# Kernel optimization log

Hardware: AMD Instinct MI355X
Metric: run time of the kernel (lower is better)

## Reference

```python
import jax, jax.numpy as jnp
import numpy as np

V, E, H, K = 50000, 256, 256, 16   # vocab, embed_dim, bi_lstm_hidden, n_tags (E must equal H)
HD = H // 2                        # per-direction hidden
B, NSEG, S = 32, 8, 128            # batch, segments, segment size
T = NSEG * S


def _lstm_dir(x, mask, Wih, Whh, b, h0, c0, reverse):
    """Masked (packed-equivalent) unidirectional LSTM. x:[T,B,E], mask:[T,B]."""
    def step(carry, inp):
        h, c = carry
        xt, mt = inp
        g = xt @ Wih.T + h @ Whh.T + b
        i, f, gg, o = jnp.split(g, 4, axis=-1)  # torch gate order i,f,g,o
        cn = jax.nn.sigmoid(f) * c + jax.nn.sigmoid(i) * jnp.tanh(gg)
        hn = jax.nn.sigmoid(o) * jnp.tanh(cn)
        m = mt[:, None]
        return (jnp.where(m, hn, h), jnp.where(m, cn, c)), jnp.where(m, hn, 0.0)
    (hT, cT), out = jax.lax.scan(step, (h0, c0), (x, mask), reverse=reverse)
    return out, (hT, cT)


def _bilstm(x, lengths, pf, pb, init=None):
    """pack_padded_sequence-equivalent BiLSTM. x:[T,B,E], lengths:[B]."""
    Tt, Bb = x.shape[0], x.shape[1]
    mask = jnp.arange(Tt)[:, None] < lengths[None, :]
    z = jnp.zeros((Bb, HD), x.dtype)
    h0f, c0f, h0b, c0b = init if init is not None else (z, z, z, z)
    of, (hf, cf) = _lstm_dir(x, mask, pf[0], pf[1], pf[2], h0f, c0f, False)
    ob, (hb, cb) = _lstm_dir(x, mask, pb[0], pb[1], pb[2], h0b, c0b, True)
    return jnp.concatenate([of, ob], -1), (hf, cf, hb, cb)


def _viterbi(emission, mask, start, trans, end):
    """torchcrf-style masked Viterbi decode. emission:[T,B,K], mask:[T,B]."""
    score = start[None, :] + emission[0]  # [B,K]
    def step(sc, inp):
        em, m = inp
        allsc = sc[:, :, None] + trans[None, :, :] + em[:, None, :]  # [B,K,K]
        best = jnp.max(allsc, axis=1)
        idx = jnp.argmax(allsc, axis=1).astype(jnp.int32)
        return jnp.where(m[:, None], best, sc), idx
    final, hist = jax.lax.scan(step, score, (emission[1:], mask[1:]))
    final = final + end[None, :]
    best_score = jnp.max(final, axis=-1)                 # [B]
    last = jnp.argmax(final, axis=-1).astype(jnp.int32)  # [B]
    def back(cur, inp):
        h, m = inp  # h:[B,K] backpointers at step t, m = mask[t+1]
        prev = jnp.take_along_axis(h, cur[:, None], axis=1)[:, 0]
        cur = jnp.where(m, prev, cur)
        return cur, cur
    _, tags_rev = jax.lax.scan(back, last, (hist, mask[1:]), reverse=True)
    tags = jnp.concatenate([tags_rev, last[None]], axis=0)  # [T,B]
    return tags, best_score


def _forward(texts, lengths, emb_table, Wih_f, Whh_f, bih_f, bhh_f,
             Wih_b, Whh_b, bih_b, bhh_b, Wlin, blin,
             crf_start, crf_trans, crf_end):
    pf = (Wih_f, Whh_f, bih_f + bhh_f)
    pb = (Wih_b, Whh_b, bih_b + bhh_b)
    emb = emb_table[texts]                      # [B,NSEG,S,E]
    x = jnp.transpose(emb, (1, 2, 0, 3))        # [NSEG,S,B,E]
    lens_seg = lengths.T                        # [NSEG,B]
    # pass 1: independent BiLSTM per segment (zero init state)
    outs, hids = jax.vmap(lambda xs, ls: _bilstm(xs, ls, pf, pb))(x, lens_seg)
    # positions >= per-segment max length are the raw embeddings (torch.cat with pad_text)
    maxlen = jnp.max(lens_seg, axis=1)          # [NSEG]
    over = jnp.arange(S)[None, :, None] >= maxlen[:, None, None]  # [NSEG,S,1]
    outs = jnp.where(over[..., None], x, outs)  # relies on E == 2*HD == H
    lstm1 = outs.reshape(NSEG * S, B, H)        # torch.cat(outputs, dim=0) -> [T,B,H]
    # get_text_lengths: per sample, valid tokens of all segments first, then pad tokens
    t_idx = jnp.arange(T)
    seg, pos = t_idx // S, t_idx % S
    valid = pos[None, :] < lengths[:, seg]                 # [B,T]
    key2 = jnp.where(valid, t_idx[None, :], t_idx[None, :] + T)
    perm = jnp.argsort(key2, axis=1)                       # [B,T] stable reorder
    lstm1_bt = jnp.transpose(lstm1, (1, 0, 2))             # [B,T,H]
    lstm2_in = jnp.transpose(
        jnp.take_along_axis(lstm1_bt, perm[..., None], axis=1), (1, 0, 2))  # [T,B,H]
    new_len = jnp.sum(lengths, axis=1)                     # [B]
    # pass 2: same LSTM weights, init state = final hidden of LAST segment (self.hidden)
    hf, cf, hb, cb = hids
    init = (hf[-1], cf[-1], hb[-1], cb[-1])
    lstm2_out, _ = _bilstm(lstm2_in, new_len, pf, pb, init)
    emission = lstm2_out @ Wlin.T + blin[None, None, :]    # [T,B,K]
    mask = jnp.arange(T)[:, None] < new_len[None, :]       # [T,B]
    return _viterbi(emission, mask, crf_start, crf_trans, crf_end)


def setup_inputs() -> dict:
    key = jax.random.key(0)
    ks = jax.random.split(key, 16)
    def u(k, shape, n):
        s = 1.0 / np.sqrt(n)
        return jax.random.uniform(k, shape, jnp.float32, -s, s)
    return {
        "texts": jax.random.randint(ks[0], (B, NSEG, S), 0, V).astype(jnp.int32),
        "lengths": jax.random.randint(ks[1], (B, NSEG), 1, S + 1).astype(jnp.int32),
        "emb_table": jax.random.normal(ks[2], (V, E), jnp.float32),
        "Wih_f": u(ks[3], (4 * HD, E), HD), "Whh_f": u(ks[4], (4 * HD, HD), HD),
        "bih_f": u(ks[5], (4 * HD,), HD), "bhh_f": u(ks[6], (4 * HD,), HD),
        "Wih_b": u(ks[7], (4 * HD, E), HD), "Whh_b": u(ks[8], (4 * HD, HD), HD),
        "bih_b": u(ks[9], (4 * HD,), HD), "bhh_b": u(ks[10], (4 * HD,), HD),
        "Wlin": u(ks[11], (K, H), H), "blin": u(ks[12], (K,), H),
        "crf_start": jax.random.uniform(ks[13], (K,), jnp.float32, -0.1, 0.1),
        "crf_trans": jax.random.uniform(ks[14], (K, K), jnp.float32, -0.1, 0.1),
        "crf_end": jax.random.uniform(ks[15], (K,), jnp.float32, -0.1, 0.1),
    }


def reference(texts, lengths, emb_table, Wih_f, Whh_f, bih_f, bhh_f,
              Wih_b, Whh_b, bih_b, bhh_b, Wlin, blin,
              crf_start, crf_trans, crf_end):
    # returns (tags [T,B] int32 padded with last tag beyond each length, viterbi score [B])
    return _forward(texts, lengths, emb_table, Wih_f, Whh_f, bih_f, bhh_f,
                    Wih_b, Whh_b, bih_b, bhh_b, Wlin, blin,
                    crf_start, crf_trans, crf_end)
```

## Files before the change

kernel.cpp:

```cpp
#include <hip/hip_runtime.h>
#include <cstdint>
#include <cstddef>


#define B_    32
#define NSEG_ 8
#define S_    128
#define T_    1024
#define E_    256
#define HD_   128
#define G_    512
#define K_    16
#define KS_   8

#define PIN4(v) asm volatile("" : "+v"((v).x), "+v"((v).y), "+v"((v).z), "+v"((v).w))

__global__ void prep_kernel(const int* __restrict__ lengths,
                            int* __restrict__ seg_off, int* __restrict__ new_len,
                            const float* __restrict__ bih_f, const float* __restrict__ bhh_f,
                            const float* __restrict__ bih_b, const float* __restrict__ bhh_b,
                            float* __restrict__ bias1,
                            const float* __restrict__ Wih_f, const float* __restrict__ Wih_b,
                            float* __restrict__ WT1)
{
    int gtid = blockIdx.x * blockDim.x + threadIdx.x;
    if (gtid < B_) {
        int acc = 0;
        for (int s = 0; s < NSEG_; s++) { seg_off[gtid*NSEG_ + s] = acc; acc += lengths[gtid*NSEG_ + s]; }
        new_len[gtid] = acc;
    }
    if (gtid < 512)       bias1[gtid] = bih_f[gtid] + bhh_f[gtid];
    else if (gtid < 1024) bias1[gtid] = bih_b[gtid-512] + bhh_b[gtid-512];
    for (int e = gtid; e < 256*1024; e += gridDim.x * blockDim.x) {
        int k = e >> 10, j = e & 1023;
        WT1[e] = (j < 512) ? Wih_f[j*E_ + k] : Wih_b[(j-512)*E_ + k];
    }
}

template <int MODE>
__global__ void __launch_bounds__(256, 4)
proj_kernel(const int* __restrict__ texts, const float* __restrict__ emb,
            const float* __restrict__ WT1, const float* __restrict__ bias1,
            const float* __restrict__ lstm_packed, float* __restrict__ xproj,
            const int* __restrict__ seg_off, const int* __restrict__ new_len)
{
    int b  = blockIdx.z;
    int nl = new_len[b];
    int p0 = blockIdx.x * 32;
    if (p0 >= nl) return;
    int j0 = blockIdx.y * 256;

    __shared__ __align__(16) float As[32][256];
    __shared__ const float* rowp[32];
    int tid = threadIdx.x;
    if (tid < 32) {
        int p = p0 + tid;
        const float* r = emb;
        if (p < nl) {
            if (MODE == 0) {
                int sg = 0;
                #pragma unroll
                for (int q = 1; q < NSEG_; q++) if (seg_off[b*NSEG_ + q] <= p) sg = q;
                int t   = p - seg_off[b*NSEG_ + sg];
                int tok = texts[(b*NSEG_ + sg)*S_ + t];
                r = emb + (size_t)tok * E_;
            } else {
                r = lstm_packed + ((size_t)b*T_ + p) * 256;
            }
        }
        rowp[tid] = r;
    }
    __syncthreads();
    #pragma unroll 4
    for (int i = 0; i < 32; i++) As[i][tid] = rowp[i][tid];
    __syncthreads();

    int pg = tid >> 6;
    int jg = tid & 63;
    int j  = j0 + jg*4;
    float acc[8][4];
    #pragma unroll
    for (int i = 0; i < 8; i++) { acc[i][0]=0.f; acc[i][1]=0.f; acc[i][2]=0.f; acc[i][3]=0.f; }

    const float* wbase = WT1 + j;
    for (int k = 0; k < 256; k += 4) {
        float4 w0 = *(const float4*)(wbase + (size_t)(k+0)*1024);
        float4 w1 = *(const float4*)(wbase + (size_t)(k+1)*1024);
        float4 w2 = *(const float4*)(wbase + (size_t)(k+2)*1024);
        float4 w3 = *(const float4*)(wbase + (size_t)(k+3)*1024);
        #pragma unroll
        for (int i = 0; i < 8; i++) {
            float4 a = *(const float4*)&As[pg*8 + i][k];
            acc[i][0] = fmaf(a.w, w3.x, fmaf(a.z, w2.x, fmaf(a.y, w1.x, fmaf(a.x, w0.x, acc[i][0]))));
            acc[i][1] = fmaf(a.w, w3.y, fmaf(a.z, w2.y, fmaf(a.y, w1.y, fmaf(a.x, w0.y, acc[i][1]))));
            acc[i][2] = fmaf(a.w, w3.z, fmaf(a.z, w2.z, fmaf(a.y, w1.z, fmaf(a.x, w0.z, acc[i][2]))));
            acc[i][3] = fmaf(a.w, w3.w, fmaf(a.z, w2.w, fmaf(a.y, w1.w, fmaf(a.x, w0.w, acc[i][3]))));
        }
    }
    float4 bs = *(const float4*)(bias1 + j);
    #pragma unroll
    for (int i = 0; i < 8; i++) {
        int p = p0 + pg*8 + i;
        if (p < nl) {
            float4 r;
            r.x = acc[i][0] + bs.x; r.y = acc[i][1] + bs.y;
            r.z = acc[i][2] + bs.z; r.w = acc[i][3] + bs.w;
            *(float4*)(xproj + (((size_t)b*T_ + p) << 10) + j) = r;
        }
    }
}

__device__ __forceinline__ float sig_f(float x) { return 1.0f / (1.0f + __expf(-x)); }
__device__ __forceinline__ float tanh_f(float x) {
    float xc = fminf(fmaxf(x, -15.0f), 15.0f);
    float e  = __expf(-2.0f * xc);
    return (1.0f - e) / (1.0f + e);
}

__device__ __forceinline__ void lstm_chain(
    const float* __restrict__ Whh,
    const float* __restrict__ xp,
    float* __restrict__ outp,
    int p_base, int len, int dir, int rev,
    const float* __restrict__ h0, const float* __restrict__ c0,
    float* __restrict__ hT, float* __restrict__ cT)
{
    __shared__ __align__(16) float  h_sh[HD_];
    __shared__ __align__(16) float4 psum[4*HD_];
    int t = threadIdx.x;
    int j = t & 127, q = t >> 7;

    float4 w[4][8];
    #pragma unroll
    for (int g = 0; g < 4; g++) {
        const float4* wr = (const float4*)(Whh + (size_t)(j + 128*g) * HD_ + 32*q);
        #pragma unroll
        for (int i = 0; i < 8; i++) { w[g][i] = wr[i]; PIN4(w[g][i]); }
    }

    float c_reg = 0.0f;
    if (t < HD_) {
        h_sh[t] = h0 ? h0[t] : 0.0f;
        c_reg   = c0 ? c0[t] : 0.0f;
    }
    __syncthreads();

    const float* xcol = xp + dir * G_ + j;
    const int    oco  = dir * HD_ + j;

    float xvi[KS_], xvf[KS_], xvg[KS_], xvo[KS_], hbuf[KS_];

    for (int gs = 0; gs < len; gs += KS_) {
        if (t < HD_) {
            if (gs > 0) {
                #pragma unroll
                for (int u = 0; u < KS_; u++) {
                    int s = gs - KS_ + u;
                    int p = p_base + (rev ? (len - 1 - s) : s);
                    outp[(size_t)p * 256 + oco] = hbuf[u];
                }
            }
            #pragma unroll
            for (int u = 0; u < KS_; u++) {
                int s = gs + u;
                if (s < len) {
                    int p = p_base + (rev ? (len - 1 - s) : s);
                    const float* r = xcol + ((size_t)p << 10);
                    xvi[u] = r[0]; xvf[u] = r[128]; xvg[u] = r[256]; xvo[u] = r[384];
                }
            }
        }
        #pragma unroll
        for (int u = 0; u < KS_; u++) {
            if (gs + u < len) {
                const float4* hv = (const float4*)h_sh + q * 8;
                float4 a0 = make_float4(0.f,0.f,0.f,0.f);
                float4 a1 = a0, a2 = a0, a3 = a0;
                #pragma unroll
                for (int i = 0; i < 8; i++) {
                    float4 h4 = hv[i];
                    a0.x = fmaf(h4.x, w[0][i].x, a0.x); a0.y = fmaf(h4.y, w[0][i].y, a0.y);
                    a0.z = fmaf(h4.z, w[0][i].z, a0.z); a0.w = fmaf(h4.w, w[0][i].w, a0.w);
                    a1.x = fmaf(h4.x, w[1][i].x, a1.x); a1.y = fmaf(h4.y, w[1][i].y, a1.y);
                    a1.z = fmaf(h4.z, w[1][i].z, a1.z); a1.w = fmaf(h4.w, w[1][i].w, a1.w);
                    a2.x = fmaf(h4.x, w[2][i].x, a2.x); a2.y = fmaf(h4.y, w[2][i].y, a2.y);
                    a2.z = fmaf(h4.z, w[2][i].z, a2.z); a2.w = fmaf(h4.w, w[2][i].w, a2.w);
                    a3.x = fmaf(h4.x, w[3][i].x, a3.x); a3.y = fmaf(h4.y, w[3][i].y, a3.y);
                    a3.z = fmaf(h4.z, w[3][i].z, a3.z); a3.w = fmaf(h4.w, w[3][i].w, a3.w);
                }
                psum[q*128 + j] = make_float4((a0.x+a0.y)+(a0.z+a0.w),
                                              (a1.x+a1.y)+(a1.z+a1.w),
                                              (a2.x+a2.y)+(a2.z+a2.w),
                                              (a3.x+a3.y)+(a3.z+a3.w));
                __syncthreads();
                if (t < HD_) {
                    float4 p0 = psum[j], p1 = psum[128 + j], p2 = psum[256 + j], p3 = psum[384 + j];
                    float gi = xvi[u] + ((p0.x + p1.x) + (p2.x + p3.x));
                    float gf = xvf[u] + ((p0.y + p1.y) + (p2.y + p3.y));
                    float gg = xvg[u] + ((p0.z + p1.z) + (p2.z + p3.z));
                    float go = xvo[u] + ((p0.w + p1.w) + (p2.w + p3.w));
                    float cn = sig_f(gf) * c_reg + sig_f(gi) * tanh_f(gg);
                    c_reg = cn;
                    float hn = sig_f(go) * tanh_f(cn);
                    h_sh[j] = hn;
                    hbuf[u] = hn;
                }
                __syncthreads();
            }
        }
    }
    if (t < HD_ && len > 0) {
        int gs = ((len - 1) / KS_) * KS_;
        #pragma unroll
        for (int u = 0; u < KS_; u++) {
            int s = gs + u;
            if (s < len) {
                int p = p_base + (rev ? (len - 1 - s) : s);
                outp[(size_t)p * 256 + oco] = hbuf[u];
            }
        }
    }
    if (hT != nullptr && t < HD_) { hT[t] = h_sh[t]; cT[t] = c_reg; }
}

__global__ void __launch_bounds__(512, 2)
lstm1_kernel(const int* __restrict__ lengths, const int* __restrict__ seg_off,
             const float* __restrict__ Whh_f, const float* __restrict__ Whh_b,
             const float* __restrict__ xproj, float* __restrict__ lstm_packed,
             float* __restrict__ hinit, float* __restrict__ cinit)
{
    int cid = blockIdx.x;
    int b = cid >> 4, seg = (cid >> 1) & 7, dir = cid & 1;
    int len = lengths[b*NSEG_ + seg];
    int pb  = seg_off[b*NSEG_ + seg];
    const float* Whh = dir ? Whh_b : Whh_f;
    float* hT = nullptr; float* cT = nullptr;
    if (seg == NSEG_ - 1) {
        hT = hinit + (dir*B_ + b)*HD_;
        cT = cinit + (dir*B_ + b)*HD_;
    }
    lstm_chain(Whh, xproj + ((size_t)b << 20), lstm_packed + (size_t)b*T_*256,
               pb, len, dir, dir, nullptr, nullptr, hT, cT);
}

__global__ void __launch_bounds__(512, 2)
lstm2_kernel(const int* __restrict__ new_len,
             const float* __restrict__ Whh_f, const float* __restrict__ Whh_b,
             const float* __restrict__ xproj, float* __restrict__ lstm_packed,
             const float* __restrict__ hinit, const float* __restrict__ cinit)
{
    int cid = blockIdx.x;
    int b = cid >> 1, dir = cid & 1;
    int len = new_len[b];
    const float* Whh = dir ? Whh_b : Whh_f;
    lstm_chain(Whh, xproj + ((size_t)b << 20), lstm_packed + (size_t)b*T_*256,
               0, len, dir, dir,
               hinit + (dir*B_ + b)*HD_, cinit + (dir*B_ + b)*HD_,
               nullptr, nullptr);
}

__global__ void __launch_bounds__(256)
emission_kernel(const float* __restrict__ lstm_packed, const float* __restrict__ Wlin,
                const float* __restrict__ blin, float* __restrict__ emis,
                const int* __restrict__ new_len)
{
    int b  = blockIdx.y;
    int nl = new_len[b];
    int p0 = blockIdx.x * 16;
    if (p0 >= nl) return;
    int pl = threadIdx.x >> 4, s = threadIdx.x & 15;
    int p  = p0 + pl;
    const float4* xr = (const float4*)(lstm_packed + ((size_t)b*T_ + p) * 256);
    const float4* wr = (const float4*)(Wlin + (size_t)s * 256);
    float ax = 0.f, ay = 0.f, az = 0.f, aw = 0.f;
    #pragma unroll
    for (int i = 0; i < 64; i++) {
        float4 a = xr[i]; float4 ww = wr[i];
        ax = fmaf(a.x, ww.x, ax); ay = fmaf(a.y, ww.y, ay);
        az = fmaf(a.z, ww.z, az); aw = fmaf(a.w, ww.w, aw);
    }
    if (p < nl) emis[((size_t)b*T_ + p)*K_ + s] = (ax + ay) + (az + aw) + blin[s];
}

__global__ void __launch_bounds__(64)
viterbi_kernel(const float* __restrict__ emis, const float* __restrict__ start,
               const float* __restrict__ trans, const float* __restrict__ endv,
               const int* __restrict__ new_len, float* __restrict__ out)
{
    int b    = blockIdx.x;
    int nl   = new_len[b];
    int lane = threadIdx.x;
    int s    = lane & 15, q4 = lane >> 4;

    __shared__ unsigned char hist[T_ * K_];
    __shared__ unsigned char tagb[T_];

    float tr[4];
    #pragma unroll
    for (int jj = 0; jj < 4; jj++) tr[jj] = trans[(q4*4 + jj)*K_ + s];

    const float* em = emis + (size_t)b * T_ * K_;
    float sc = start[s] + em[s];

    for (int p = 1; p < nl; p++) {
        float e = em[p*K_ + s];
        float m = -3.4e38f; int a = 0;
        #pragma unroll
        for (int jj = 0; jj < 4; jj++) {
            int q   = q4*4 + jj;
            float sq = __shfl(sc, q, 16);
            float v  = sq + tr[jj];
            if (v > m) { m = v; a = q; }
        }
        #pragma unroll
        for (int d = 16; d < 64; d <<= 1) {
            float mo = __shfl_xor(m, d);
            int   ao = __shfl_xor(a, d);
            if (mo > m || (mo == m && ao < a)) { m = mo; a = ao; }
        }
        sc = m + e;
        if (lane < K_) hist[p*K_ + s] = (unsigned char)a;
    }

    float m = sc + endv[s]; int a = s;
    #pragma unroll
    for (int d = 1; d < 16; d <<= 1) {
        float mo = __shfl_xor(m, d);
        int   ao = __shfl_xor(a, d);
        if (mo > m || (mo == m && ao < a)) { m = mo; a = ao; }
    }
    int last = a;
    if (lane == 0) out[T_*B_ + b] = m;
    __syncthreads();

    for (int i = lane; i < T_; i += 64) tagb[i] = (unsigned char)last;
    __syncthreads();
    if (lane == 0) {
        int cur = last;
        for (int j = nl - 2; j >= 0; j--) {
            cur = hist[(j+1)*K_ + cur];
            tagb[j] = (unsigned char)cur;
        }
    }
    __syncthreads();
    for (int i = lane; i < T_; i += 64) out[(size_t)i*B_ + b] = (float)tagb[i];
}

extern "C" void kernel_launch(void* const* d_in, const int* in_sizes, int n_in,
                              void* d_out, int out_size, void* d_ws, size_t ws_size,
                              hipStream_t stream)
{
    (void)in_sizes; (void)n_in; (void)out_size; (void)ws_size;
    const int*   texts   = (const int*)  d_in[0];
    const int*   lengths = (const int*)  d_in[1];
    const float* emb     = (const float*)d_in[2];
    const float* Wih_f   = (const float*)d_in[3];
    const float* Whh_f   = (const float*)d_in[4];
    const float* bih_f   = (const float*)d_in[5];
    const float* bhh_f   = (const float*)d_in[6];
    const float* Wih_b   = (const float*)d_in[7];
    const float* Whh_b   = (const float*)d_in[8];
    const float* bih_b   = (const float*)d_in[9];
    const float* bhh_b   = (const float*)d_in[10];
    const float* Wlin    = (const float*)d_in[11];
    const float* blin    = (const float*)d_in[12];
    const float* c_start = (const float*)d_in[13];
    const float* c_trans = (const float*)d_in[14];
    const float* c_end   = (const float*)d_in[15];
    float* out = (float*)d_out;

    char* w = (char*)d_ws;
    int*   seg_off     = (int*)(w);
    int*   new_len     = (int*)(w + 1024);
    float* bias1       = (float*)(w + 4096);
    float* WT1         = (float*)(w + 8192);
    float* hinit       = (float*)(w + 8192 + 1048576);
    float* cinit       = hinit + 8192;
    float* lstm_packed = cinit + 8192;
    float* xproj       = lstm_packed + (size_t)B_*T_*256;
    float* emis        = xproj + ((size_t)B_ << 20);

    prep_kernel<<<128, 256, 0, stream>>>(lengths, seg_off, new_len,
                                         bih_f, bhh_f, bih_b, bhh_b, bias1,
                                         Wih_f, Wih_b, WT1);
    proj_kernel<0><<<dim3(32, 4, B_), 256, 0, stream>>>(texts, emb, WT1, bias1,
                                                        lstm_packed, xproj, seg_off, new_len);
    lstm1_kernel<<<512, 512, 0, stream>>>(lengths, seg_off, Whh_f, Whh_b,
                                          xproj, lstm_packed, hinit, cinit);
    proj_kernel<1><<<dim3(32, 4, B_), 256, 0, stream>>>(texts, emb, WT1, bias1,
                                                        lstm_packed, xproj, seg_off, new_len);
    lstm2_kernel<<<64, 512, 0, stream>>>(new_len, Whh_f, Whh_b,
                                         xproj, lstm_packed, hinit, cinit);
    emission_kernel<<<dim3(64, B_), 256, 0, stream>>>(lstm_packed, Wlin, blin, emis, new_len);
    viterbi_kernel<<<B_, 64, 0, stream>>>(emis, c_start, c_trans, c_end, new_len, out);
}
```

Before: 1.582 ms.

## Interleave gate columns and prefetch next chunk of input projections in LSTM

The gate layout of the input projection weights and bias is permuted so the four gates of each hidden unit are contiguous, which lets the recurrent loop fetch all four gate inputs with a single 16-byte load. Loads for the next chunk of time steps are issued ahead with inline assembly and waited on by explicit vmcnt counters, so their latency overlaps the current chunk's serial compute. Hidden outputs are now stored immediately at each step rather than buffered. This relies on hand-managed waitcnt ordering, where a wrong count could read stale registers.

```diff
diff --git a/kernel.cpp b/kernel.cpp
--- a/kernel.cpp
+++ b/kernel.cpp
@@ -15,6 +15,17 @@
 
 #define PIN4(v) asm volatile("" : "+v"((v).x), "+v"((v).y), "+v"((v).z), "+v"((v).w))
 
+__device__ __forceinline__ float4 gload4(const float* p) {
+    float4 d;
+    asm volatile("global_load_dwordx4 %0, %1, off"
+                 : "=v"(d) : "v"((unsigned long long)(uintptr_t)p));
+    return d;
+}
+__device__ __forceinline__ void gstore1(float* p, float v) {
+    asm volatile("global_store_dword %0, %1, off"
+                 :: "v"((unsigned long long)(uintptr_t)p), "v"(v));
+}
+
 __global__ void prep_kernel(const int* __restrict__ lengths,
                             int* __restrict__ seg_off, int* __restrict__ new_len,
                             const float* __restrict__ bih_f, const float* __restrict__ bhh_f,
@@ -29,11 +40,16 @@
         for (int s = 0; s < NSEG_; s++) { seg_off[gtid*NSEG_ + s] = acc; acc += lengths[gtid*NSEG_ + s]; }
         new_len[gtid] = acc;
     }
-    if (gtid < 512)       bias1[gtid] = bih_f[gtid] + bhh_f[gtid];
-    else if (gtid < 1024) bias1[gtid] = bih_b[gtid-512] + bhh_b[gtid-512];
+    if (gtid < 1024) {
+        int dir = gtid >> 9, w = gtid & 511, j = w >> 2, g = w & 3;
+        int r = g * HD_ + j;
+        bias1[gtid] = dir ? (bih_b[r] + bhh_b[r]) : (bih_f[r] + bhh_f[r]);
+    }
     for (int e = gtid; e < 256*1024; e += gridDim.x * blockDim.x) {
-        int k = e >> 10, j = e & 1023;
-        WT1[e] = (j < 512) ? Wih_f[j*E_ + k] : Wih_b[(j-512)*E_ + k];
+        int k = e >> 10, jcol = e & 1023;
+        int dir = jcol >> 9, w = jcol & 511, j = w >> 2, g = w & 3;
+        int r = g * HD_ + j;
+        WT1[e] = dir ? Wih_b[(size_t)r*E_ + k] : Wih_f[(size_t)r*E_ + k];
     }
 }
 
@@ -145,28 +161,31 @@
     }
     __syncthreads();
 
-    const float* xcol = xp + dir * G_ + j;
-    const int    oco  = dir * HD_ + j;
-
-    float xvi[KS_], xvf[KS_], xvg[KS_], xvo[KS_], hbuf[KS_];
+    const float* xbase = xp + dir * G_ + 4 * j;
+    float*       obase = outp + dir * HD_ + j;
+
+    float4 xc[KS_], xn[KS_];
+
+    if (t < HD_ && len > 0) {
+        #pragma unroll
+        for (int u = 0; u < KS_; u++) {
+            int s = u < len ? u : len - 1;
+            int p = p_base + (rev ? (len - 1 - s) : s);
+            xn[u] = gload4(xbase + ((size_t)p << 10));
+        }
+    }
+    asm volatile("s_waitcnt vmcnt(0)");
 
     for (int gs = 0; gs < len; gs += KS_) {
         if (t < HD_) {
-            if (gs > 0) {
+            #pragma unroll
+            for (int u = 0; u < KS_; u++) { PIN4(xn[u]); xc[u] = xn[u]; }
+            if (gs + KS_ < len) {
                 #pragma unroll
                 for (int u = 0; u < KS_; u++) {
-                    int s = gs - KS_ + u;
+                    int s = gs + KS_ + u; s = s < len ? s : len - 1;
                     int p = p_base + (rev ? (len - 1 - s) : s);
-                    outp[(size_t)p * 256 + oco] = hbuf[u];
-                }
-            }
-            #pragma unroll
-            for (int u = 0; u < KS_; u++) {
-                int s = gs + u;
-                if (s < len) {
-                    int p = p_base + (rev ? (len - 1 - s) : s);
-                    const float* r = xcol + ((size_t)p << 10);
-                    xvi[u] = r[0]; xvf[u] = r[128]; xvg[u] = r[256]; xvo[u] = r[384];
+                    xn[u] = gload4(xbase + ((size_t)p << 10));
                 }
             }
         }
@@ -195,32 +214,25 @@
                 __syncthreads();
                 if (t < HD_) {
                     float4 p0 = psum[j], p1 = psum[128 + j], p2 = psum[256 + j], p3 = psum[384 + j];
-                    float gi = xvi[u] + ((p0.x + p1.x) + (p2.x + p3.x));
-                    float gf = xvf[u] + ((p0.y + p1.y) + (p2.y + p3.y));
-                    float gg = xvg[u] + ((p0.z + p1.z) + (p2.z + p3.z));
-                    float go = xvo[u] + ((p0.w + p1.w) + (p2.w + p3.w));
+                    float gi = xc[u].x + ((p0.x + p1.x) + (p2.x + p3.x));
+                    float gf = xc[u].y + ((p0.y + p1.y) + (p2.y + p3.y));
+                    float gg = xc[u].z + ((p0.z + p1.z) + (p2.z + p3.z));
+                    float go = xc[u].w + ((p0.w + p1.w) + (p2.w + p3.w));
                     float cn = sig_f(gf) * c_reg + sig_f(gi) * tanh_f(gg);
                     c_reg = cn;
                     float hn = sig_f(go) * tanh_f(cn);
                     h_sh[j] = hn;
-                    hbuf[u] = hn;
+                    int s = gs + u;
+                    int p = p_base + (rev ? (len - 1 - s) : s);
+                    gstore1(obase + (size_t)p * 256, hn);
                 }
                 __syncthreads();
             }
         }
-    }
-    if (t < HD_ && len > 0) {
-        int gs = ((len - 1) / KS_) * KS_;
-        #pragma unroll
-        for (int u = 0; u < KS_; u++) {
-            int s = gs + u;
-            if (s < len) {
-                int p = p_base + (rev ? (len - 1 - s) : s);
-                outp[(size_t)p * 256 + oco] = hbuf[u];
-            }
-        }
+        asm volatile("s_waitcnt vmcnt(8)");
     }
     if (hT != nullptr && t < HD_) { hT[t] = h_sh[t]; cT[t] = c_reg; }
+    asm volatile("s_waitcnt vmcnt(0)");
 }
 
 __global__ void __launch_bounds__(512, 2)
```

Measured after the change: 1.624 ms. 1.03x slower.
